# Optimization experiments

Hardware: AMD Instinct MI355X
Metric: run time of the kernel (lower is better)

Reference implementation:

```python
import jax, jax.numpy as jnp
import numpy as np

BETA = 0.1
EPS_LOW = 0.2
EPS_HIGH = 0.2
TEMPERATURE = 1.0


def setup_inputs() -> dict:
    key = jax.random.key(0)
    ks = jax.random.split(key, 6)
    B, T, H, V = 4, 1024, 2048, 32000
    x = jax.random.normal(ks[0], (B, T, H), dtype=jnp.float32)
    ref_input = jax.random.normal(ks[1], (B, T, H), dtype=jnp.float32)
    W = jax.random.normal(ks[2], (V, H), dtype=jnp.float32) * (1.0 / np.sqrt(H))
    ref_W = jax.random.normal(ks[3], (V, H), dtype=jnp.float32) * (1.0 / np.sqrt(H))
    selected_token_ids = jax.random.randint(ks[4], (B, T), 0, V, dtype=jnp.int64)
    attention_mask = jnp.ones((B, T), dtype=jnp.float32)
    advantages = jax.random.normal(ks[5], (B,), dtype=jnp.float32)
    return {
        "x": x,
        "W": W,
        "ref_W": ref_W,
        "ref_input": ref_input,
        "selected_token_ids": selected_token_ids,
        "attention_mask": attention_mask,
        "advantages": advantages,
    }


def _per_token_logps_and_mean(h, W, ids):
    # h: [B,T,H], W: [V,H] -> logits [B,T,V]
    logits = jnp.einsum("bth,vh->btv", h, W)
    if TEMPERATURE != 1.0:
        logits = logits / TEMPERATURE
    log_probs = jax.nn.log_softmax(logits, axis=-1)
    ptl = jnp.take_along_axis(log_probs, ids[..., None], axis=-1)[..., 0]
    return ptl, log_probs.mean()


def reference(x, W, ref_W, ref_input, selected_token_ids, attention_mask, advantages):
    per_token_logps, log_probs_mean = _per_token_logps_and_mean(x, W, selected_token_ids)

    # reference model path (no grad)
    ref_per_token_logps, _ = _per_token_logps_and_mean(
        jax.lax.stop_gradient(ref_input), jax.lax.stop_gradient(ref_W), selected_token_ids
    )
    ref_per_token_logps = jax.lax.stop_gradient(ref_per_token_logps)

    old_per_token_logps = jax.lax.stop_gradient(per_token_logps)
    coef_1 = jnp.exp(per_token_logps - old_per_token_logps)
    coef_2 = jnp.clip(coef_1, 1.0 - EPS_LOW, 1.0 + EPS_HIGH)
    adv = advantages[:, None]  # [B,1]
    per_token_loss = -jnp.minimum(coef_1 * adv, coef_2 * adv)

    delta = ref_per_token_logps - per_token_logps
    kl_div = jnp.exp(delta) - delta - 1.0
    per_token_loss = per_token_loss + BETA * kl_div

    loss = (per_token_loss * attention_mask).sum() / jnp.clip(attention_mask.sum(), 1.0)

    kl_metric = ((kl_div * attention_mask).sum(axis=1) / jnp.clip(attention_mask.sum(axis=1), 1.0)).mean()
    return loss, per_token_logps.mean(), log_probs_mean, kl_metric
```

## Files before the change

### kernel.cpp

```cpp
#include <hip/hip_runtime.h>
#include <stdint.h>

#define M_TOK 4096
#define N_VOC 32000
#define K_DIM 2048
#define BM 256
#define BN 256
#define BK 64
#define NT (K_DIM / BK)
#define BETA 0.1f
#define W_SCALE 32.0f
#define INV_W_SCALE (1.0f / 32.0f)

typedef float f32x4 __attribute__((ext_vector_type(4)));

__global__ __launch_bounds__(256) void cast_f32_fp8(const float* __restrict__ in,
                                                    unsigned* __restrict__ out, int n4,
                                                    float scale) {
  int i = blockIdx.x * blockDim.x + threadIdx.x;
  int stride = gridDim.x * blockDim.x;
  const float4* __restrict__ in4 = (const float4*)in;
  for (; i < n4; i += stride) {
    float4 f = in4[i];
    int v = __builtin_amdgcn_cvt_pk_fp8_f32(f.x * scale, f.y * scale, 0, false);
    v = __builtin_amdgcn_cvt_pk_fp8_f32(f.z * scale, f.w * scale, v, true);
    out[i] = (unsigned)v;
  }
}

__global__ __launch_bounds__(512, 2) void gemm_stats(
    const unsigned char* __restrict__ A,
    const unsigned char* __restrict__ B,
    const int* __restrict__ ids,
    float* __restrict__ S, float* __restrict__ L, float* __restrict__ sel) {
  __shared__ unsigned char lds[65536];

  const int tid = threadIdx.x;
  const int w = tid >> 6;
  const int l = tid & 63;
  const int m0 = blockIdx.y * BM;
  const int n0 = blockIdx.x * BN;
  const int wm = w >> 2, wn = w & 3;
  const int l15 = l & 15, quad = l >> 4;

  const unsigned char* pA = A + (size_t)(m0 + w * 32 + (l >> 1)) * K_DIM + (l & 1) * 16;
  const unsigned char* pB = B + (size_t)(n0 + w * 32 + (l >> 1)) * K_DIM + (l & 1) * 16;
  unsigned char* ldsA = &lds[w * 1024];
  unsigned char* ldsB = &lds[16384 + w * 1024];

  const int ra = (wm * 128 + l15) * 32 + quad * 8;
  const int rb = 16384 + (wn * 64 + l15) * 32 + quad * 8;

  f32x4 acc[8][4];
  const f32x4 zero = {0.f, 0.f, 0.f, 0.f};
#pragma unroll
  for (int i = 0; i < 8; ++i)
#pragma unroll
    for (int j = 0; j < 4; ++j) acc[i][j] = zero;

#define STAGE(nb, p, kn)                                                                 \
  do {                                                                                   \
    __builtin_amdgcn_global_load_lds(                                                    \
        (const __attribute__((address_space(1))) unsigned int*)(pA + (kn) + (p) * 32),   \
        (__attribute__((address_space(3))) unsigned int*)(ldsA + (nb) * 32768 + (p) * 8192), \
        16, 0, 0);                                                                       \
    __builtin_amdgcn_global_load_lds(                                                    \
        (const __attribute__((address_space(1))) unsigned int*)(pB + (kn) + (p) * 32),   \
        (__attribute__((address_space(3))) unsigned int*)(ldsB + (nb) * 32768 + (p) * 8192), \
        16, 0, 0);                                                                       \
  } while (0)

#define PHASE(bf, p)                                                                     \
  do {                                                                                   \
    const unsigned char* Ab = &lds[(bf) * 32768 + (p) * 8192] + ra;                      \
    const unsigned char* Bb = &lds[(bf) * 32768 + (p) * 8192] + rb;                      \
    long long af[8], bq[4];                                                              \
    _Pragma("unroll") for (int i = 0; i < 8; ++i)                                        \
        af[i] = *(const long long*)(Ab + i * 512);                                       \
    _Pragma("unroll") for (int j = 0; j < 4; ++j)                                        \
        bq[j] = *(const long long*)(Bb + j * 512);                                       \
    __builtin_amdgcn_s_setprio(1);                                                       \
    _Pragma("unroll") for (int i = 0; i < 8; ++i)                                        \
      _Pragma("unroll") for (int j = 0; j < 4; ++j)                                      \
        acc[i][j] = __builtin_amdgcn_mfma_f32_16x16x32_fp8_fp8(af[i], bq[j],             \
                                                               acc[i][j], 0, 0, 0);      \
    __builtin_amdgcn_s_setprio(0);                                                       \
  } while (0)

  STAGE(0, 0, 0);
  STAGE(0, 1, 0);

  for (int t = 0; t < NT - 1; ++t) {
    const int bf = t & 1, nb = bf ^ 1;
    const int kn = (t + 1) * BK;
    STAGE(nb, 0, kn);
    asm volatile("s_waitcnt vmcnt(4)" ::: "memory");
    __builtin_amdgcn_s_barrier();
    asm volatile("" ::: "memory");
    PHASE(bf, 0);
    STAGE(nb, 1, kn);
    asm volatile("s_waitcnt vmcnt(4)" ::: "memory");
    __builtin_amdgcn_s_barrier();
    asm volatile("" ::: "memory");
    PHASE(bf, 1);
  }
  asm volatile("s_waitcnt vmcnt(2)" ::: "memory");
  __builtin_amdgcn_s_barrier();
  asm volatile("" ::: "memory");
  PHASE(1, 0);
  asm volatile("s_waitcnt vmcnt(0)" ::: "memory");
  __builtin_amdgcn_s_barrier();
  asm volatile("" ::: "memory");
  PHASE(1, 1);

#undef STAGE
#undef PHASE

#pragma unroll
  for (int i = 0; i < 8; ++i) {
#pragma unroll
    for (int r = 0; r < 4; ++r) {
      int row = m0 + wm * 128 + i * 16 + quad * 4 + r;
      int sid = ids[row];
      int loc = sid - n0 - wn * 64;
      bool hit = (loc >= 0) && (loc < 64) && ((loc & 15) == l15);
      float es = 0.f, ls = 0.f, selv = 0.f;
#pragma unroll
      for (int j = 0; j < 4; ++j) {
        float v = acc[i][j][r] * INV_W_SCALE;
        es += __expf(v);
        ls += v;
        if (hit && ((loc >> 4) == j)) selv = v;
      }
      if (hit) sel[row] = selv;
#pragma unroll
      for (int mk = 1; mk < 16; mk <<= 1) {
        es += __shfl_xor(es, mk);
        ls += __shfl_xor(ls, mk);
      }
      if (l15 == 0) {
        atomicAdd(&S[row], es);
        atomicAdd(&L[row], ls);
      }
    }
  }
}

__global__ __launch_bounds__(1024) void finalize_kernel(
    const float* __restrict__ S1, const float* __restrict__ L1, const float* __restrict__ P1,
    const float* __restrict__ S2, const float* __restrict__ P2,
    const float* __restrict__ mask, const float* __restrict__ adv, float* __restrict__ out) {
  __shared__ float red[12];
  int tid = threadIdx.x;
  int lane = tid & 63;
  if (tid < 12) red[tid] = 0.f;
  __syncthreads();

  float loss_num = 0.f, mask_sum = 0.f, ptl_sum = 0.f, lpm_sum = 0.f;
  float klb[4] = {0.f, 0.f, 0.f, 0.f}, mb[4] = {0.f, 0.f, 0.f, 0.f};
#pragma unroll
  for (int k = 0; k < 4; ++k) {
    int t = k * 1024 + tid;
    float lse1 = logf(S1[t]);
    float ptl = P1[t] - lse1;
    float ref_ptl = P2[t] - logf(S2[t]);
    float d = ref_ptl - ptl;
    float kl = expf(d) - d - 1.f;
    float m = mask[t];
    float a = adv[k];
    loss_num += (-a + BETA * kl) * m;
    mask_sum += m;
    ptl_sum += ptl;
    lpm_sum += L1[t] * (1.f / (float)N_VOC) - lse1;
    klb[k] += kl * m;
    mb[k] += m;
  }
  float vals[12] = {loss_num, mask_sum, ptl_sum, lpm_sum,
                    klb[0], klb[1], klb[2], klb[3],
                    mb[0],  mb[1],  mb[2],  mb[3]};
#pragma unroll
  for (int v = 0; v < 12; ++v) {
    float xv = vals[v];
#pragma unroll
    for (int mk = 32; mk >= 1; mk >>= 1) xv += __shfl_xor(xv, mk);
    if (lane == 0) atomicAdd(&red[v], xv);
  }
  __syncthreads();
  if (tid == 0) {
    float loss = red[0] / fmaxf(red[1], 1.f);
    float km = 0.f;
#pragma unroll
    for (int b = 0; b < 4; ++b) km += red[4 + b] / fmaxf(red[8 + b], 1.f);
    out[0] = loss;
    out[1] = red[2] * (1.f / 4096.f);
    out[2] = red[3] * (1.f / 4096.f);
    out[3] = km * 0.25f;
  }
}

extern "C" void kernel_launch(void* const* d_in, const int* in_sizes, int n_in,
                              void* d_out, int out_size, void* d_ws, size_t ws_size,
                              hipStream_t stream) {
  const float* x = (const float*)d_in[0];
  const float* W = (const float*)d_in[1];
  const float* ref_W = (const float*)d_in[2];
  const float* ref_x = (const float*)d_in[3];
  const int* ids = (const int*)d_in[4];
  const float* mask = (const float*)d_in[5];
  const float* adv = (const float*)d_in[6];
  float* out = (float*)d_out;

  char* ws = (char*)d_ws;
  unsigned char* Wq = (unsigned char*)ws;
  unsigned char* xq = (unsigned char*)(ws + (size_t)N_VOC * K_DIM);
  float* accum = (float*)(ws + (size_t)N_VOC * K_DIM + (size_t)M_TOK * K_DIM);
  float* S1 = accum;
  float* L1 = accum + 4096;
  float* P1 = accum + 8192;
  float* S2 = accum + 12288;
  float* L2 = accum + 16384;
  float* P2 = accum + 20480;

  hipMemsetAsync(accum, 0, 6 * 4096 * sizeof(float), stream);

  dim3 grid(N_VOC / BN, M_TOK / BM);

  cast_f32_fp8<<<2048, 256, 0, stream>>>(W, (unsigned*)Wq, N_VOC * K_DIM / 4, W_SCALE);
  cast_f32_fp8<<<512, 256, 0, stream>>>(x, (unsigned*)xq, M_TOK * K_DIM / 4, 1.0f);
  gemm_stats<<<grid, 512, 0, stream>>>(xq, Wq, ids, S1, L1, P1);

  cast_f32_fp8<<<2048, 256, 0, stream>>>(ref_W, (unsigned*)Wq, N_VOC * K_DIM / 4, W_SCALE);
  cast_f32_fp8<<<512, 256, 0, stream>>>(ref_x, (unsigned*)xq, M_TOK * K_DIM / 4, 1.0f);
  gemm_stats<<<grid, 512, 0, stream>>>(xq, Wq, ids, S2, L2, P2);

  finalize_kernel<<<1, 1024, 0, stream>>>(S1, L1, P1, S2, P2, mask, adv, out);
}
```

Measured before the change: 2.040 ms.

## Swizzle LDS tile layout and halve barriers per K-step in FP8 GEMM

Changes the global-to-LDS staging so each wave loads full 64-byte K rows into an XOR-swizzled LDS layout. Fragment reads use a matching swizzled offset, which is meant to remove LDS bank conflicts on the ds_read_b64 fragment loads. The main loop also drops from two barriers per K tile to one, with A and B staged between the two MFMA phases. The trade-off is a full vmcnt(0) wait each iteration, which may expose more global-load latency than the earlier split pipeline.

```diff
diff --git a/kernel.cpp b/kernel.cpp
--- a/kernel.cpp
+++ b/kernel.cpp
@@ -43,13 +43,18 @@
   const int wm = w >> 2, wn = w & 3;
   const int l15 = l & 15, quad = l >> 4;
 
-  const unsigned char* pA = A + (size_t)(m0 + w * 32 + (l >> 1)) * K_DIM + (l & 1) * 16;
-  const unsigned char* pB = B + (size_t)(n0 + w * 32 + (l >> 1)) * K_DIM + (l & 1) * 16;
-  unsigned char* ldsA = &lds[w * 1024];
-  unsigned char* ldsB = &lds[16384 + w * 1024];
-
-  const int ra = (wm * 128 + l15) * 32 + quad * 8;
-  const int rb = 16384 + (wn * 64 + l15) * 32 + quad * 8;
+  const int srow = l >> 2;
+  const int sc = (l & 3) ^ (srow & 3) ^ ((srow >> 2) & 3);
+  const size_t sOff = (size_t)srow * K_DIM + (size_t)(sc * 16);
+  const unsigned char* pA = A + (size_t)(m0 + w * 32) * K_DIM + sOff;
+  const unsigned char* pB = B + (size_t)(n0 + w * 32) * K_DIM + sOff;
+  const size_t RS16 = (size_t)16 * K_DIM;
+
+  unsigned char* dA = &lds[w * 2048];
+  unsigned char* dB = &lds[16384 + w * 2048];
+
+  const int sw = (l15 & 3) ^ ((l15 >> 2) & 3);
+  const int roff = l15 * 64 + (((quad >> 1) ^ sw) << 4) + (quad & 1) * 8;
 
   f32x4 acc[8][4];
   const f32x4 zero = {0.f, 0.f, 0.f, 0.f};
@@ -58,62 +63,64 @@
 #pragma unroll
     for (int j = 0; j < 4; ++j) acc[i][j] = zero;
 
-#define STAGE(nb, p, kn)                                                                 \
-  do {                                                                                   \
-    __builtin_amdgcn_global_load_lds(                                                    \
-        (const __attribute__((address_space(1))) unsigned int*)(pA + (kn) + (p) * 32),   \
-        (__attribute__((address_space(3))) unsigned int*)(ldsA + (nb) * 32768 + (p) * 8192), \
-        16, 0, 0);                                                                       \
-    __builtin_amdgcn_global_load_lds(                                                    \
-        (const __attribute__((address_space(1))) unsigned int*)(pB + (kn) + (p) * 32),   \
-        (__attribute__((address_space(3))) unsigned int*)(ldsB + (nb) * 32768 + (p) * 8192), \
-        16, 0, 0);                                                                       \
+#define GLL(src, dst)                                                              \
+  __builtin_amdgcn_global_load_lds(                                                \
+      (const __attribute__((address_space(1))) unsigned int*)(src),                \
+      (__attribute__((address_space(3))) unsigned int*)(dst), 16, 0, 0)
+
+#define STAGE_A(nb, kn)                                                            \
+  do {                                                                            \
+    GLL(pA + (kn), dA + (nb)*32768);                                              \
+    GLL(pA + (kn) + RS16, dA + (nb)*32768 + 1024);                                \
   } while (0)
 
-#define PHASE(bf, p)                                                                     \
-  do {                                                                                   \
-    const unsigned char* Ab = &lds[(bf) * 32768 + (p) * 8192] + ra;                      \
-    const unsigned char* Bb = &lds[(bf) * 32768 + (p) * 8192] + rb;                      \
-    long long af[8], bq[4];                                                              \
-    _Pragma("unroll") for (int i = 0; i < 8; ++i)                                        \
-        af[i] = *(const long long*)(Ab + i * 512);                                       \
-    _Pragma("unroll") for (int j = 0; j < 4; ++j)                                        \
-        bq[j] = *(const long long*)(Bb + j * 512);                                       \
-    __builtin_amdgcn_s_setprio(1);                                                       \
-    _Pragma("unroll") for (int i = 0; i < 8; ++i)                                        \
-      _Pragma("unroll") for (int j = 0; j < 4; ++j)                                      \
-        acc[i][j] = __builtin_amdgcn_mfma_f32_16x16x32_fp8_fp8(af[i], bq[j],             \
-                                                               acc[i][j], 0, 0, 0);      \
-    __builtin_amdgcn_s_setprio(0);                                                       \
+#define STAGE_B(nb, kn)                                                            \
+  do {                                                                            \
+    GLL(pB + (kn), dB + (nb)*32768);                                              \
+    GLL(pB + (kn) + RS16, dB + (nb)*32768 + 1024);                                \
   } while (0)
 
-  STAGE(0, 0, 0);
-  STAGE(0, 1, 0);
+#define PHASE(bf, p)                                                               \
+  do {                                                                            \
+    const unsigned char* Abase = &lds[(bf)*32768 + wm*8192];                       \
+    const unsigned char* Bbase = &lds[(bf)*32768 + 16384 + wn*4096];               \
+    const int ro = roff ^ ((p) << 5);                                              \
+    long long af[8], bq[4];                                                        \
+    _Pragma("unroll") for (int i = 0; i < 8; ++i)                                  \
+        af[i] = *(const long long*)(Abase + i * 1024 + ro);                        \
+    _Pragma("unroll") for (int j = 0; j < 4; ++j)                                  \
+        bq[j] = *(const long long*)(Bbase + j * 1024 + ro);                        \
+    __builtin_amdgcn_s_setprio(1);                                                 \
+    _Pragma("unroll") for (int i = 0; i < 8; ++i)                                  \
+      _Pragma("unroll") for (int j = 0; j < 4; ++j)                                \
+        acc[i][j] = __builtin_amdgcn_mfma_f32_16x16x32_fp8_fp8(af[i], bq[j],       \
+                                                               acc[i][j], 0, 0, 0);\
+    __builtin_amdgcn_s_setprio(0);                                                 \
+  } while (0)
+
+  STAGE_A(0, 0);
+  STAGE_B(0, 0);
 
   for (int t = 0; t < NT - 1; ++t) {
     const int bf = t & 1, nb = bf ^ 1;
     const int kn = (t + 1) * BK;
-    STAGE(nb, 0, kn);
-    asm volatile("s_waitcnt vmcnt(4)" ::: "memory");
+    asm volatile("s_waitcnt vmcnt(0)" ::: "memory");
     __builtin_amdgcn_s_barrier();
     asm volatile("" ::: "memory");
+    STAGE_A(nb, kn);
     PHASE(bf, 0);
-    STAGE(nb, 1, kn);
-    asm volatile("s_waitcnt vmcnt(4)" ::: "memory");
-    __builtin_amdgcn_s_barrier();
-    asm volatile("" ::: "memory");
+    STAGE_B(nb, kn);
     PHASE(bf, 1);
   }
-  asm volatile("s_waitcnt vmcnt(2)" ::: "memory");
+  asm volatile("s_waitcnt vmcnt(0)" ::: "memory");
   __builtin_amdgcn_s_barrier();
   asm volatile("" ::: "memory");
   PHASE(1, 0);
-  asm volatile("s_waitcnt vmcnt(0)" ::: "memory");
-  __builtin_amdgcn_s_barrier();
-  asm volatile("" ::: "memory");
   PHASE(1, 1);
 
-#undef STAGE
+#undef GLL
+#undef STAGE_A
+#undef STAGE_B
 #undef PHASE
 
 #pragma unroll
```

Result: faster. 1.745 ms (-14.4%).
